# Performance work log

Hardware: AMD Instinct MI355X
Metric: run time of the kernel (lower is better)

Reference implementation:

```python
import jax, jax.numpy as jnp
import numpy as np

B, L, E = 2, 8192, 1024
H, D = 16, 64          # num_heads, head_dim
W, G = 512, 64         # window_size, group_size


def _rope(x):
    # x: [B, H, S, D]. Faithful to original (with the obvious pe-indexing fix):
    # pe[:,0::2]=sin(pos*inv_freq), pe[:,1::2]=cos(pos*inv_freq)
    S, Dh = x.shape[-2], x.shape[-1]
    pos = jnp.arange(S, dtype=jnp.float32)[:, None]                     # [S,1]
    inv_freq = 1.0 / (10000.0 ** (jnp.arange(0, Dh, 2, dtype=jnp.float32) / Dh))
    ang = pos * inv_freq                                                # [S, D/2]
    sin, cos = jnp.sin(ang), jnp.cos(ang)
    xe, xo = x[..., 0::2], x[..., 1::2]
    # cat(even_rotated, odd_rotated) along last dim, as in original
    return jnp.concatenate([xe * sin + xo * cos, -xe * cos + xo * sin], axis=-1)


def setup_inputs() -> dict:
    key = jax.random.key(0)
    ks = jax.random.split(key, 11)
    s = 0.02  # keep pre-softmax logits well-scaled
    return {
        "query": jax.random.normal(ks[0], (B, L, E), jnp.float32),
        "key":   jax.random.normal(ks[1], (B, L, E), jnp.float32),
        "value": jax.random.normal(ks[2], (B, L, E), jnp.float32),
        "Wq": jax.random.normal(ks[3], (E, E), jnp.float32) * s,
        "bq": jax.random.normal(ks[4], (E,), jnp.float32) * s,
        "Wk": jax.random.normal(ks[5], (E, E), jnp.float32) * s,
        "bk": jax.random.normal(ks[6], (E,), jnp.float32) * s,
        "Wv": jax.random.normal(ks[7], (E, E), jnp.float32) * s,
        "bv": jax.random.normal(ks[8], (E,), jnp.float32) * s,
        "Wo": jax.random.normal(ks[9], (E, E), jnp.float32) * s,
        "bo": jax.random.normal(ks[10], (E,), jnp.float32) * s,
    }


def reference(query, key, value, Wq, bq, Wk, bk, Wv, bv, Wo, bo):
    Bq, Lq, _ = query.shape
    Lk = key.shape[1]
    # projections (torch Linear: x @ W.T + b), split heads -> [B, H, L, D]
    def proj(x, Wt, b):
        y = x @ Wt.T + b
        return y.reshape(Bq, -1, H, D).transpose(0, 2, 1, 3)
    q = _rope(proj(query, Wq, bq))
    k = _rope(proj(key, Wk, bk))
    v = proj(value, Wv, bv)

    # sliding-window grouped scores: for each group starting at idx=n*G,
    # score against keys[idx : min(idx+W, Lk)], zero-fill the tail.
    n_groups = Lq // G
    starts = jnp.arange(n_groups) * G                                    # [N]
    kidx = starts[:, None] + jnp.arange(W)[None, :]                      # [N, W]
    valid = kidx < Lk                                                    # [N, W]
    kidx_c = jnp.minimum(kidx, Lk - 1)
    k_blk = k[:, :, kidx_c]                                              # [B,H,N,W,D]
    q_grp = q.reshape(Bq, H, n_groups, G, D)                             # [B,H,N,G,D]
    scores = jnp.einsum('bhngd,bhnwd->bhngw', q_grp, k_blk) / (D ** 0.5)
    scores = jnp.where(valid[None, None, :, None, :], scores, 0.0)       # zero-fill tail
    scores = scores.reshape(Bq, H, Lq, W)                                # [B,H,Lq,W]

    probs = jax.nn.softmax(scores, axis=-1)                              # softmax over W incl. zeros (faithful)
    ctx = jnp.einsum('bhqw,bhwd->bhqd', probs, v[:, :, :W])              # faithful: first-W values only
    ctx = ctx.transpose(0, 2, 1, 3).reshape(Bq, Lq, H * D)
    return ctx @ Wo.T + bo
```

## Files before the change

kernel.cpp:

```cpp
#include <hip/hip_runtime.h>


typedef unsigned short ushort_t;
typedef __attribute__((ext_vector_type(8))) __bf16 bf16x8;
typedef __attribute__((ext_vector_type(4))) float f32x4;
typedef __attribute__((ext_vector_type(8))) unsigned short ushort8;
typedef __attribute__((ext_vector_type(4))) unsigned int u32x4;

#define MFMA16(a, b, c) __builtin_amdgcn_mfma_f32_16x16x32_bf16((a), (b), (c), 0, 0, 0)

static __device__ __forceinline__ ushort_t f2bf(float f) {
    unsigned u = __float_as_uint(f);
    u += 0x7fffu + ((u >> 16) & 1u);
    return (ushort_t)(u >> 16);
}

static __device__ __forceinline__ ushort_t f2bfc(float f) {
    __bf16 h = (__bf16)f;
    return __builtin_bit_cast(ushort_t, h);
}

typedef __attribute__((address_space(3))) unsigned int lds_u32;
typedef const __attribute__((address_space(1))) unsigned int glb_u32;

static __device__ __forceinline__ void gload_lds16(const void* g, void* l) {
    __builtin_amdgcn_global_load_lds((glb_u32*)g, (lds_u32*)l, 16, 0, 0);
}

__global__ __launch_bounds__(256) void cvt_bf16(const float* __restrict__ in,
                                                ushort_t* __restrict__ out, long n8) {
    long i = (long)blockIdx.x * 256 + threadIdx.x;
    if (i >= n8) return;
    const float4* p = (const float4*)in + i * 2;
    float4 a = p[0], b = p[1];
    ushort8 o;
    o[0] = f2bf(a.x); o[1] = f2bf(a.y); o[2] = f2bf(a.z); o[3] = f2bf(a.w);
    o[4] = f2bf(b.x); o[5] = f2bf(b.y); o[6] = f2bf(b.z); o[7] = f2bf(b.w);
    *(ushort8*)(out + i * 8) = o;
}

__global__ __launch_bounds__(256) void cvt_w4(const float* __restrict__ w0,
                                              const float* __restrict__ w1,
                                              const float* __restrict__ w2,
                                              const float* __restrict__ w3,
                                              ushort_t* __restrict__ o0,
                                              ushort_t* __restrict__ o1,
                                              ushort_t* __restrict__ o2,
                                              ushort_t* __restrict__ o3) {
    int wsel = blockIdx.x >> 9;
    const float* in = (wsel == 0) ? w0 : (wsel == 1) ? w1 : (wsel == 2) ? w2 : w3;
    ushort_t* out = (wsel == 0) ? o0 : (wsel == 1) ? o1 : (wsel == 2) ? o2 : o3;
    long i = (long)(blockIdx.x & 511) * 256 + threadIdx.x;
    const float4* p = (const float4*)in + i * 2;
    float4 a = p[0], b = p[1];
    ushort8 o;
    o[0] = f2bf(a.x); o[1] = f2bf(a.y); o[2] = f2bf(a.z); o[3] = f2bf(a.w);
    o[4] = f2bf(b.x); o[5] = f2bf(b.y); o[6] = f2bf(b.z); o[7] = f2bf(b.w);
    *(ushort8*)(out + i * 8) = o;
}

__global__ __launch_bounds__(256) void cvt_value(const float* __restrict__ in,
                                                 ushort_t* __restrict__ out) {
    int i = blockIdx.x * 256 + threadIdx.x;
    int f = i * 8;
    int m = f >> 10, c = f & 1023;
    long src = ((long)(m >> 9) * 8192 + (m & 511)) * 1024 + c;
    const float4* p = (const float4*)(in + src);
    float4 a = p[0], b = p[1];
    ushort8 o;
    o[0] = f2bf(a.x); o[1] = f2bf(a.y); o[2] = f2bf(a.z); o[3] = f2bf(a.w);
    o[4] = f2bf(b.x); o[5] = f2bf(b.y); o[6] = f2bf(b.z); o[7] = f2bf(b.w);
    *(ushort8*)(out + f) = o;
}

__global__ __launch_bounds__(256) void rope_tab(float2* __restrict__ tab) {
    int i = blockIdx.x * 256 + threadIdx.x;
    int l = i >> 5, j = i & 31;
    float inv = exp2f(-(float)j * 0.4152410118609203f);
    float a = (float)l * inv;
    tab[i] = make_float2(sinf(a), cosf(a));
}

template <int MODE>
__global__ __launch_bounds__(256) void gemm_bt(const ushort_t* __restrict__ A,
                                               const ushort_t* __restrict__ Bw,
                                               const float* __restrict__ bias,
                                               void* __restrict__ outp,
                                               const float2* __restrict__ rope,
                                               float oscale) {
    __shared__ __align__(16) ushort_t sA[128 * 32];
    __shared__ __align__(16) ushort_t sB[128 * 32];
    const int tid = threadIdx.x, lane = tid & 63, wv = tid >> 6;
    const int wr = wv >> 1, wc = wv & 1;
    const long bm = (long)blockIdx.x * 128;
    const int bn = blockIdx.y * 128;

    f32x4 acc[4][4] = {};

    const int srow = tid >> 2;
    const int sslot = tid & 3;
    const int ca = sslot ^ (srow & 3);
    const ushort_t* Ab = A + (bm + srow) * 1024 + ca * 8;
    const ushort_t* Bb = Bw + (long)(bn + srow) * 1024 + ca * 8;
    ushort_t* la = &sA[srow * 32 + sslot * 8];
    ushort_t* lb = &sB[srow * 32 + sslot * 8];

    for (int kt = 0; kt < 32; ++kt) {
        const int ko = kt * 32;
        gload_lds16(Ab + ko, la);
        gload_lds16(Ab + 64 * 1024 + ko, la + 64 * 32);
        gload_lds16(Bb + ko, lb);
        gload_lds16(Bb + 64 * 1024 + ko, lb + 64 * 32);
        __syncthreads();
        bf16x8 af[4], bfr[4];
#pragma unroll
        for (int mt = 0; mt < 4; ++mt) {
            int r = wr * 64 + mt * 16 + (lane & 15);
            int sl = (lane >> 4) ^ (r & 3);
            af[mt] = *(const bf16x8*)&sA[r * 32 + sl * 8];
        }
#pragma unroll
        for (int nt = 0; nt < 4; ++nt) {
            int r = wc * 64 + nt * 16 + (lane & 15);
            int sl = (lane >> 4) ^ (r & 3);
            bfr[nt] = *(const bf16x8*)&sB[r * 32 + sl * 8];
        }
#pragma unroll
        for (int mt = 0; mt < 4; ++mt)
#pragma unroll
            for (int nt = 0; nt < 4; ++nt)
                acc[mt][nt] = MFMA16(af[mt], bfr[nt], acc[mt][nt]);
        __syncthreads();
    }

    if constexpr (MODE == 2) {
        float* out = (float*)outp;
#pragma unroll
        for (int nt = 0; nt < 4; ++nt) {
            int col = bn + wc * 64 + nt * 16 + (lane & 15);
            float bs = bias[col];
#pragma unroll
            for (int mt = 0; mt < 4; ++mt) {
                long g0 = bm + wr * 64 + mt * 16 + ((lane >> 4) << 2);
#pragma unroll
                for (int r = 0; r < 4; ++r)
                    out[(g0 + r) * 1024 + col] = acc[mt][nt][r] + bs;
            }
        }
    } else if constexpr (MODE == 1) {
        __shared__ __align__(16) ushort_t sE[4][4096];
        ushort_t* out = (ushort_t*)outp;
        ushort_t* se = &sE[wv][0];
#pragma unroll
        for (int nt = 0; nt < 4; ++nt) {
            int col = bn + wc * 64 + nt * 16 + (lane & 15);
            float bs = bias[col];
            int c = (col & 63) >> 1;
            int outd = ((col & 1) ? 32 : 0) + c;
            int chunk = outd >> 3, dlo = outd & 7;
#pragma unroll
            for (int mt = 0; mt < 4; ++mt) {
#pragma unroll
                for (int r = 0; r < 4; ++r) {
                    float y = acc[mt][nt][r] + bs;
                    float yp = __shfl_xor(y, 1);
                    int row = mt * 16 + ((lane >> 4) << 2) + r;
                    int l = ((int)bm + wr * 64 + row) & 8191;
                    float2 sc = rope[l * 32 + c];
                    float val = ((col & 1) ? (y * sc.x - yp * sc.y)
                                           : (y * sc.x + yp * sc.y)) * oscale;
                    se[row * 64 + ((chunk ^ (row & 7)) << 3) + dlo] = f2bf(val);
                }
            }
        }
        asm volatile("s_waitcnt lgkmcnt(0)" ::: "memory");
        int hh = (bn + wc * 64) >> 6;
#pragma unroll
        for (int i = 0; i < 8; ++i) {
            int row = i * 8 + (lane >> 3);
            int cb = lane & 7;
            ushort8 vv = *(const ushort8*)&se[row * 64 + ((cb ^ (row & 7)) << 3)];
            int m = (int)bm + wr * 64 + row;
            int bb = m >> 13, l = m & 8191;
            *(ushort8*)&out[(((long)(bb * 16 + hh)) * 8192 + l) * 64 + cb * 8] = vv;
        }
    } else {
        ushort_t* out = (ushort_t*)outp;
#pragma unroll
        for (int nt = 0; nt < 4; ++nt) {
            int col = bn + wc * 64 + nt * 16 + (lane & 15);
            float bs = bias[col];
            int hh = col >> 6, d = col & 63;
#pragma unroll
            for (int mt = 0; mt < 4; ++mt) {
                int m0 = (int)bm + wr * 64 + mt * 16 + ((lane >> 4) << 2);
#pragma unroll
                for (int r = 0; r < 4; ++r) {
                    int m = m0 + r;
                    int bb = m >> 9, w = m & 511;
                    int t = w & 31;
                    int s = (t < 16) ? ((t >> 2) * 8 + (t & 3))
                                     : (((t & 15) >> 2) * 8 + 4 + (t & 3));
                    int wp = (w & ~31) | s;
                    out[(((long)(bb * 16 + hh)) * 64 + d) * 512 + wp] =
                        f2bf(acc[mt][nt][r] + bs);
                }
            }
        }
    }
}

__global__ __launch_bounds__(256) void attn(const ushort_t* __restrict__ qr,
                                            const ushort_t* __restrict__ kr,
                                            const ushort_t* __restrict__ vT,
                                            ushort_t* __restrict__ ctx) {
    __shared__ __align__(16) ushort_t sK[512 * 64];
    __shared__ __align__(16) ushort_t sE[4][1024];
    const int bid = blockIdx.x;
    const int gc = bid & 15, h = (bid >> 4) & 15, b = bid >> 8;
    const int tid = threadIdx.x, lane = tid & 63, wv = tid >> 6;

    const f32x4 kZero = {0.f, 0.f, 0.f, 0.f};
    const u32x4 kOneU = {0x3F803F80u, 0x3F803F80u, 0x3F803F80u, 0x3F803F80u};
    const bf16x8 vone = __builtin_bit_cast(bf16x8, kOneU);

    const ushort_t* khead = kr + ((long)(b * 16 + h)) * 8192 * 64;
    const ushort_t* qhead = qr + ((long)(b * 16 + h)) * 8192 * 64;
    const ushort_t* vb = vT + ((long)(b * 16 + h)) * 64 * 512;

    {
        const long base = (long)gc * 512;
#pragma unroll
        for (int i = 0; i < 16; ++i) {
            int idx = i * 256 + tid;
            int row = idx >> 3, sl = idx & 7;
            int chunk = sl ^ (row & 7);
            gload_lds16(khead + (base + row) * 64 + chunk * 8,
                        (char*)sK + idx * 16);
        }
    }
    __syncthreads();

    ushort_t* se = &sE[wv][0];

#pragma unroll 1
    for (int gi = 0; gi < 8; ++gi) {
        const int g = gc * 8 + gi;
        const int start = g * 64;
        const int climit = 8192 - start;
        const int kclim = climit >> 5;

        const int qrow = start + wv * 16 + (lane & 15);
        const ushort_t* qp = qhead + (long)qrow * 64 + ((lane >> 4) * 8);
        bf16x8 aq0 = *(const bf16x8*)qp;
        bf16x8 aq1 = *(const bf16x8*)(qp + 32);

        f32x4 o[4];
#pragma unroll
        for (int d0 = 0; d0 < 4; ++d0) o[d0] = kZero;
        float ssum = 0.f;

#pragma unroll
        for (int kc = 0; kc < 16; ++kc) {
            if (kc == 2) {
                __syncthreads();
                if (gi < 7) {
#pragma unroll
                    for (int i = 0; i < 2; ++i) {
                        int idx = i * 256 + tid;
                        int rrel = idx >> 3, sl = idx & 7;
                        long rg = (long)start + 512 + rrel;
                        int chunk = sl ^ ((int)rg & 7);
                        long rc = rg > 8191 ? 8191 : rg;
                        gload_lds16(khead + rc * 64 + chunk * 8,
                                    (char*)sK + (start & 511) * 128 + idx * 16);
                    }
                }
            }
            bf16x8 pa;
            if (kc < kclim) {
                int c0 = kc * 32 + (lane & 15);
                int c1 = c0 + 16;
                int slot0 = (start + c0) & 511, x0 = slot0 & 7;
                int slot1 = (start + c1) & 511, x1 = slot1 & 7;
                bf16x8 kb00 = *(const bf16x8*)&sK[slot0 * 64 + (((lane >> 4)) ^ x0) * 8];
                bf16x8 kb01 = *(const bf16x8*)&sK[slot0 * 64 + ((4 + (lane >> 4)) ^ x0) * 8];
                bf16x8 kb10 = *(const bf16x8*)&sK[slot1 * 64 + (((lane >> 4)) ^ x1) * 8];
                bf16x8 kb11 = *(const bf16x8*)&sK[slot1 * 64 + ((4 + (lane >> 4)) ^ x1) * 8];
                __builtin_amdgcn_s_setprio(1);
                f32x4 s0 = MFMA16(kb00, aq0, kZero);
                s0 = MFMA16(kb01, aq1, s0);
                f32x4 s1 = MFMA16(kb10, aq0, kZero);
                s1 = MFMA16(kb11, aq1, s1);
                __builtin_amdgcn_s_setprio(0);

                float p0[4], p1[4];
#pragma unroll
                for (int r = 0; r < 4; ++r) {
                    p0[r] = __expf(s0[r] * 0.125f);
                    p1[r] = __expf(s1[r] * 0.125f);
                    ssum += p0[r] + p1[r];
                }
                pa[0] = (__bf16)p0[0]; pa[1] = (__bf16)p0[1];
                pa[2] = (__bf16)p0[2]; pa[3] = (__bf16)p0[3];
                pa[4] = (__bf16)p1[0]; pa[5] = (__bf16)p1[1];
                pa[6] = (__bf16)p1[2]; pa[7] = (__bf16)p1[3];
            } else {
                pa = vone;
                ssum += 8.0f;
            }
#pragma unroll
            for (int d0 = 0; d0 < 4; ++d0) {
                bf16x8 bvf = *(const bf16x8*)&vb[(long)(d0 * 16 + (lane & 15)) * 512 +
                                                 kc * 32 + (lane >> 4) * 8];
                o[d0] = MFMA16(pa, bvf, o[d0]);
            }
        }

        ssum += __shfl_xor(ssum, 16);
        ssum += __shfl_xor(ssum, 32);
        float rin = 1.0f / ssum;
        float si[4];
#pragma unroll
        for (int r = 0; r < 4; ++r)
            si[r] = __shfl(rin, ((lane >> 4) << 2) + r);

#pragma unroll
        for (int d0 = 0; d0 < 4; ++d0) {
#pragma unroll
            for (int r = 0; r < 4; ++r) {
                int row = ((lane >> 4) << 2) + r;
                int d = d0 * 16 + (lane & 15);
                se[row * 64 + (((d >> 3) ^ (row & 7)) << 3) + (d & 7)] =
                    f2bfc(o[d0][r] * si[r]);
            }
        }
        asm volatile("s_waitcnt lgkmcnt(0)" ::: "memory");
#pragma unroll
        for (int i = 0; i < 2; ++i) {
            int row = i * 8 + (lane >> 3);
            int cb = lane & 7;
            ushort8 vv = *(const ushort8*)&se[row * 64 + ((cb ^ (row & 7)) << 3)];
            int l = start + wv * 16 + row;
            *(ushort8*)&ctx[((long)(b * 8192 + l)) * 1024 + h * 64 + cb * 8] = vv;
        }
    }
}

extern "C" void kernel_launch(void* const* d_in, const int* in_sizes, int n_in,
                              void* d_out, int out_size, void* d_ws, size_t ws_size,
                              hipStream_t stream) {
    const float* query = (const float*)d_in[0];
    const float* key_ = (const float*)d_in[1];
    const float* value = (const float*)d_in[2];
    const float* Wq = (const float*)d_in[3];
    const float* bq = (const float*)d_in[4];
    const float* Wk = (const float*)d_in[5];
    const float* bk = (const float*)d_in[6];
    const float* Wv = (const float*)d_in[7];
    const float* bv = (const float*)d_in[8];
    const float* Wo = (const float*)d_in[9];
    const float* bo = (const float*)d_in[10];
    float* out = (float*)d_out;
    char* ws = (char*)d_ws;

    ushort_t* Xbf = (ushort_t*)(ws);
    ushort_t* Wqb = (ushort_t*)(ws + 33554432L);
    ushort_t* Wkb = (ushort_t*)(ws + 33554432L + 2097152L);
    ushort_t* Wvb = (ushort_t*)(ws + 33554432L + 2 * 2097152L);
    ushort_t* Wob = (ushort_t*)(ws + 33554432L + 3 * 2097152L);
    float2* rope = (float2*)(ws + 41943040L);
    ushort_t* qrb = (ushort_t*)(ws + 44040192L);
    ushort_t* krb = (ushort_t*)(ws + 77594624L);
    ushort_t* vin = (ushort_t*)(ws + 111149056L);
    ushort_t* vTb = (ushort_t*)(ws + 113246208L);

    rope_tab<<<1024, 256, 0, stream>>>(rope);
    cvt_w4<<<2048, 256, 0, stream>>>(Wq, Wk, Wv, Wo, Wqb, Wkb, Wvb, Wob);

    cvt_bf16<<<8192, 256, 0, stream>>>(query, Xbf, 2097152);
    gemm_bt<1><<<dim3(128, 8), 256, 0, stream>>>(Xbf, Wqb, bq, qrb, rope, 1.0f);
    cvt_bf16<<<8192, 256, 0, stream>>>(key_, Xbf, 2097152);
    gemm_bt<1><<<dim3(128, 8), 256, 0, stream>>>(Xbf, Wkb, bk, krb, rope, 1.0f);
    cvt_value<<<512, 256, 0, stream>>>(value, vin);
    gemm_bt<3><<<dim3(8, 8), 256, 0, stream>>>(vin, Wvb, bv, vTb, nullptr, 1.0f);

    attn<<<512, 256, 0, stream>>>(qrb, krb, vTb, Xbf);
    gemm_bt<2><<<dim3(128, 8), 256, 0, stream>>>(Xbf, Wob, bo, out, nullptr, 1.0f);
}
```

Before: 337.2 us.

## Merge prep kernels, remap GEMM block order, prefetch V fragments in attention

Combines the rope table, weight conversion and value conversion into one launch to cut kernel-launch overhead. The 128x8 GEMM grid gets remapped block indices so that groups of blocks sharing B tiles run together, aiming for better L2 reuse. In attention, the V fragments for the next chunk are loaded one iteration early to hide global load latency behind the MFMAs. The prefetch costs extra registers, which could lower occupancy.

Measured after the change: 332.3 us. No clear change (-1.5%).

```diff
diff --git a/kernel.cpp b/kernel.cpp
--- a/kernel.cpp
+++ b/kernel.cpp
@@ -39,46 +39,48 @@
     *(ushort8*)(out + i * 8) = o;
 }
 
-__global__ __launch_bounds__(256) void cvt_w4(const float* __restrict__ w0,
-                                              const float* __restrict__ w1,
-                                              const float* __restrict__ w2,
-                                              const float* __restrict__ w3,
-                                              ushort_t* __restrict__ o0,
-                                              ushort_t* __restrict__ o1,
-                                              ushort_t* __restrict__ o2,
-                                              ushort_t* __restrict__ o3) {
-    int wsel = blockIdx.x >> 9;
-    const float* in = (wsel == 0) ? w0 : (wsel == 1) ? w1 : (wsel == 2) ? w2 : w3;
-    ushort_t* out = (wsel == 0) ? o0 : (wsel == 1) ? o1 : (wsel == 2) ? o2 : o3;
-    long i = (long)(blockIdx.x & 511) * 256 + threadIdx.x;
-    const float4* p = (const float4*)in + i * 2;
-    float4 a = p[0], b = p[1];
-    ushort8 o;
-    o[0] = f2bf(a.x); o[1] = f2bf(a.y); o[2] = f2bf(a.z); o[3] = f2bf(a.w);
-    o[4] = f2bf(b.x); o[5] = f2bf(b.y); o[6] = f2bf(b.z); o[7] = f2bf(b.w);
-    *(ushort8*)(out + i * 8) = o;
-}
-
-__global__ __launch_bounds__(256) void cvt_value(const float* __restrict__ in,
-                                                 ushort_t* __restrict__ out) {
-    int i = blockIdx.x * 256 + threadIdx.x;
-    int f = i * 8;
-    int m = f >> 10, c = f & 1023;
-    long src = ((long)(m >> 9) * 8192 + (m & 511)) * 1024 + c;
-    const float4* p = (const float4*)(in + src);
-    float4 a = p[0], b = p[1];
-    ushort8 o;
-    o[0] = f2bf(a.x); o[1] = f2bf(a.y); o[2] = f2bf(a.z); o[3] = f2bf(a.w);
-    o[4] = f2bf(b.x); o[5] = f2bf(b.y); o[6] = f2bf(b.z); o[7] = f2bf(b.w);
-    *(ushort8*)(out + f) = o;
-}
-
-__global__ __launch_bounds__(256) void rope_tab(float2* __restrict__ tab) {
-    int i = blockIdx.x * 256 + threadIdx.x;
-    int l = i >> 5, j = i & 31;
-    float inv = exp2f(-(float)j * 0.4152410118609203f);
-    float a = (float)l * inv;
-    tab[i] = make_float2(sinf(a), cosf(a));
+__global__ __launch_bounds__(256) void prep(const float* __restrict__ w0,
+                                            const float* __restrict__ w1,
+                                            const float* __restrict__ w2,
+                                            const float* __restrict__ w3,
+                                            ushort_t* __restrict__ o0,
+                                            ushort_t* __restrict__ o1,
+                                            ushort_t* __restrict__ o2,
+                                            ushort_t* __restrict__ o3,
+                                            const float* __restrict__ value,
+                                            ushort_t* __restrict__ vin,
+                                            float2* __restrict__ rope) {
+    const int bid = blockIdx.x;
+    if (bid < 1024) {
+        int i = bid * 256 + threadIdx.x;
+        int l = i >> 5, j = i & 31;
+        float inv = exp2f(-(float)j * 0.4152410118609203f);
+        float a = (float)l * inv;
+        rope[i] = make_float2(sinf(a), cosf(a));
+    } else if (bid < 3072) {
+        int b2 = bid - 1024;
+        int wsel = b2 >> 9;
+        const float* in = (wsel == 0) ? w0 : (wsel == 1) ? w1 : (wsel == 2) ? w2 : w3;
+        ushort_t* out = (wsel == 0) ? o0 : (wsel == 1) ? o1 : (wsel == 2) ? o2 : o3;
+        long i = (long)(b2 & 511) * 256 + threadIdx.x;
+        const float4* p = (const float4*)in + i * 2;
+        float4 a = p[0], b = p[1];
+        ushort8 o;
+        o[0] = f2bf(a.x); o[1] = f2bf(a.y); o[2] = f2bf(a.z); o[3] = f2bf(a.w);
+        o[4] = f2bf(b.x); o[5] = f2bf(b.y); o[6] = f2bf(b.z); o[7] = f2bf(b.w);
+        *(ushort8*)(out + i * 8) = o;
+    } else {
+        int i = (bid - 3072) * 256 + threadIdx.x;
+        int f = i * 8;
+        int m = f >> 10, c = f & 1023;
+        long src = ((long)(m >> 9) * 8192 + (m & 511)) * 1024 + c;
+        const float4* p = (const float4*)(value + src);
+        float4 a = p[0], b = p[1];
+        ushort8 o;
+        o[0] = f2bf(a.x); o[1] = f2bf(a.y); o[2] = f2bf(a.z); o[3] = f2bf(a.w);
+        o[4] = f2bf(b.x); o[5] = f2bf(b.y); o[6] = f2bf(b.z); o[7] = f2bf(b.w);
+        *(ushort8*)(vin + f) = o;
+    }
 }
 
 template <int MODE>
@@ -92,8 +94,18 @@
     __shared__ __align__(16) ushort_t sB[128 * 32];
     const int tid = threadIdx.x, lane = tid & 63, wv = tid >> 6;
     const int wr = wv >> 1, wc = wv & 1;
-    const long bm = (long)blockIdx.x * 128;
-    const int bn = blockIdx.y * 128;
+
+    int bmx, bny;
+    if (gridDim.x == 128) {
+        int id = blockIdx.x + (int)(gridDim.x * blockIdx.y);
+        bmx = (id & 7) * 16 + ((id >> 3) & 15);
+        bny = id >> 7;
+    } else {
+        bmx = blockIdx.x;
+        bny = blockIdx.y;
+    }
+    const long bm = (long)bmx * 128;
+    const int bn = bny * 128;
 
     f32x4 acc[4][4] = {};
 
@@ -260,6 +272,11 @@
         for (int d0 = 0; d0 < 4; ++d0) o[d0] = kZero;
         float ssum = 0.f;
 
+        bf16x8 vf0 = *(const bf16x8*)&vb[(long)(0 * 16 + (lane & 15)) * 512 + (lane >> 4) * 8];
+        bf16x8 vf1 = *(const bf16x8*)&vb[(long)(1 * 16 + (lane & 15)) * 512 + (lane >> 4) * 8];
+        bf16x8 vf2 = *(const bf16x8*)&vb[(long)(2 * 16 + (lane & 15)) * 512 + (lane >> 4) * 8];
+        bf16x8 vf3 = *(const bf16x8*)&vb[(long)(3 * 16 + (lane & 15)) * 512 + (lane >> 4) * 8];
+
 #pragma unroll
         for (int kc = 0; kc < 16; ++kc) {
             if (kc == 2) {
@@ -276,6 +293,13 @@
                                     (char*)sK + (start & 511) * 128 + idx * 16);
                     }
                 }
+            }
+            bf16x8 vn0, vn1, vn2, vn3;
+            if (kc < 15) {
+                vn0 = *(const bf16x8*)&vb[(long)(0 * 16 + (lane & 15)) * 512 + (kc + 1) * 32 + (lane >> 4) * 8];
+                vn1 = *(const bf16x8*)&vb[(long)(1 * 16 + (lane & 15)) * 512 + (kc + 1) * 32 + (lane >> 4) * 8];
+                vn2 = *(const bf16x8*)&vb[(long)(2 * 16 + (lane & 15)) * 512 + (kc + 1) * 32 + (lane >> 4) * 8];
+                vn3 = *(const bf16x8*)&vb[(long)(3 * 16 + (lane & 15)) * 512 + (kc + 1) * 32 + (lane >> 4) * 8];
             }
             bf16x8 pa;
             if (kc < kclim) {
@@ -309,12 +333,11 @@
                 pa = vone;
                 ssum += 8.0f;
             }
-#pragma unroll
-            for (int d0 = 0; d0 < 4; ++d0) {
-                bf16x8 bvf = *(const bf16x8*)&vb[(long)(d0 * 16 + (lane & 15)) * 512 +
-                                                 kc * 32 + (lane >> 4) * 8];
-                o[d0] = MFMA16(pa, bvf, o[d0]);
-            }
+            o[0] = MFMA16(pa, vf0, o[0]);
+            o[1] = MFMA16(pa, vf1, o[1]);
+            o[2] = MFMA16(pa, vf2, o[2]);
+            o[3] = MFMA16(pa, vf3, o[3]);
+            if (kc < 15) { vf0 = vn0; vf1 = vn1; vf2 = vn2; vf3 = vn3; }
         }
 
         ssum += __shfl_xor(ssum, 16);
@@ -375,14 +398,13 @@
     ushort_t* vin = (ushort_t*)(ws + 111149056L);
     ushort_t* vTb = (ushort_t*)(ws + 113246208L);
 
-    rope_tab<<<1024, 256, 0, stream>>>(rope);
-    cvt_w4<<<2048, 256, 0, stream>>>(Wq, Wk, Wv, Wo, Wqb, Wkb, Wvb, Wob);
+    prep<<<3584, 256, 0, stream>>>(Wq, Wk, Wv, Wo, Wqb, Wkb, Wvb, Wob,
+                                   value, vin, rope);
 
     cvt_bf16<<<8192, 256, 0, stream>>>(query, Xbf, 2097152);
     gemm_bt<1><<<dim3(128, 8), 256, 0, stream>>>(Xbf, Wqb, bq, qrb, rope, 1.0f);
     cvt_bf16<<<8192, 256, 0, stream>>>(key_, Xbf, 2097152);
     gemm_bt<1><<<dim3(128, 8), 256, 0, stream>>>(Xbf, Wkb, bk, krb, rope, 1.0f);
-    cvt_value<<<512, 256, 0, stream>>>(value, vin);
     gemm_bt<3><<<dim3(8, 8), 256, 0, stream>>>(vin, Wvb, bv, vTb, nullptr, 1.0f);
 
     attn<<<512, 256, 0, stream>>>(qrb, krb, vTb, Xbf);
```
